# Kernel tuning notes

Measured on AMD Instinct MI355X. Metric: run time of the kernel, lower is better.

## Reference

```python
import jax, jax.numpy as jnp
import numpy as np

B, C, H, W = 4, 64, 256, 256
WIDE = 256      # num_features * width_multiplier
K = 4           # dynamic kernel banks
KS = 3          # kernel size
RED = 16        # channels // reduction = 64 // 4
PAD = KS // 2


def _wn(v, g):
    # torch weight_norm, dim=0: norm over all dims except leading dim
    n = jnp.sqrt(jnp.sum(v * v, axis=tuple(range(1, v.ndim)), keepdims=True))
    return g * v / n


def _conv(x, w, groups=1):
    return jax.lax.conv_general_dilated(
        x, w, window_strides=(1, 1), padding=[(PAD, PAD), (PAD, PAD)],
        feature_group_count=groups, dimension_numbers=('NCHW', 'OIHW', 'NCHW'))


def setup_inputs() -> dict:
    key = jax.random.key(0)
    ks = jax.random.split(key, 16)
    s = lambda k, shape, sc: jax.random.normal(k, shape, jnp.float32) * sc
    return {
        'x': jax.random.normal(ks[0], (B, C, H, W), jnp.float32),
        'scale': jax.random.uniform(ks[1], (B, 1), jnp.float32, 1.0, 4.0),
        # body conv 1 (weight-normed, ReLU)
        'v1': s(ks[2], (WIDE, C, KS, KS), 0.05), 'g1': jnp.ones((WIDE, 1, 1, 1), jnp.float32),
        'b1': jnp.zeros((WIDE,), jnp.float32),
        # body conv 2 (weight-normed, no act)
        'v2': s(ks[3], (C, WIDE, KS, KS), 0.05), 'g2': jnp.ones((C, 1, 1, 1), jnp.float32),
        'b2': jnp.zeros((C,), jnp.float32),
        # scale-aware dynamic conv: K banks of [C_out, C_in, k, k], weight-normed over dim 0 (=K)
        'dyn_v': s(ks[4], (K, C, C, KS, KS), 0.05), 'dyn_g': jnp.ones((K, 1, 1, 1, 1), jnp.float32),
        'dyn_b': jnp.zeros((K, C), jnp.float32),
        # routing: Linear(1 -> K) + softmax
        'att_w': s(ks[5], (1, K), 1.0), 'att_b': jnp.zeros((K,), jnp.float32),
        # SE block: Linear(C -> C/red, no bias), ReLU, Linear(C/red -> C, no bias), Sigmoid
        'se_w1': s(ks[6], (RED, C), 0.1), 'se_w2': s(ks[7], (C, RED), 0.1),
    }


def reference(x, scale, v1, g1, b1, v2, g2, b2, dyn_v, dyn_g, dyn_b,
              att_w, att_b, se_w1, se_w2):
    # --- body: wide weight-normed conv stack ---
    r = jax.nn.relu(_conv(x, _wn(v1, g1)) + b1[None, :, None, None])   # [B,WIDE,H,W]
    r = _conv(r, _wn(v2, g2)) + b2[None, :, None, None]                # [B,C,H,W]
    # --- scale-aware dynamic conv: per-sample softmax mix of K kernels ---
    att = jax.nn.softmax(scale @ att_w + att_b, axis=-1)               # [B,K]
    w_bank = _wn(dyn_v, dyn_g)                                         # [K,C,C,k,k]
    w_b = jnp.einsum('bk,koicd->boicd', att, w_bank)                   # [B,C,C,k,k]
    bias_b = att @ dyn_b                                               # [B,C]
    # batch-grouped conv: one distinct kernel per sample
    y = _conv(r.reshape(1, B * C, H, W), w_b.reshape(B * C, C, KS, KS), groups=B)
    y = y.reshape(B, C, H, W) + bias_b[:, :, None, None]
    # --- SE gating ---
    p = jnp.mean(y, axis=(2, 3))                                       # [B,C]
    gate = jax.nn.sigmoid(jax.nn.relu(p @ se_w1.T) @ se_w2.T)          # [B,C]
    y = y * gate[:, :, None, None]
    # --- residual ---
    return x + y
```

## Files before the change

kernel.cpp:

```cpp
#include <hip/hip_runtime.h>

typedef __attribute__((ext_vector_type(8))) short short8;
typedef __attribute__((ext_vector_type(4))) float f32x4;

#define HH 256
#define WW 256

__device__ inline unsigned int f2bf(float x) {
  unsigned int u = __float_as_uint(x);
  return (u + 0x7fffu + ((u >> 16) & 1u)) >> 16;
}
__device__ inline unsigned int pack2(float a, float b) {
  return f2bf(a) | (f2bf(b) << 16);
}

__global__ __launch_bounds__(256) void xpose_k(const float* __restrict__ x,
                                               unsigned short* __restrict__ xcl) {
  const int t = threadIdx.x;
  const int ci = t & 63;
  const int wv = t >> 6;
  const int x0 = blockIdx.x * 64;
  const int y  = blockIdx.y;
  const int b  = blockIdx.z;
  const float* src = x + ((size_t)(b * 64 + ci) * HH + y) * WW + x0 + wv;
  unsigned short* dst = xcl + ((size_t)(b * HH + y) * WW + x0 + wv) * 64 + ci;
#pragma unroll
  for (int k = 0; k < 16; ++k)
    dst[(size_t)k * 4 * 64] = (unsigned short)f2bf(src[4 * k]);
}

template <int COUT, int CINK>
__global__ __launch_bounds__(256) void wnorm_k(const float* __restrict__ v,
                                               const float* __restrict__ g,
                                               unsigned short* __restrict__ out) {
  constexpr int N = CINK * 9;
  const int co = blockIdx.x, t = threadIdx.x;
  const float* vb = v + (size_t)co * N;
  float s = 0.f;
  for (int i = t; i < N; i += 256) { float a = vb[i]; s += a * a; }
  for (int off = 32; off > 0; off >>= 1) s += __shfl_xor(s, off, 64);
  __shared__ float red[4];
  if ((t & 63) == 0) red[t >> 6] = s;
  __syncthreads();
  const float tot = red[0] + red[1] + red[2] + red[3];
  const float sc = g[co] / sqrtf(tot);
  for (int i = t; i < N; i += 256) {
    int ci = i / 9, tap = i - 9 * (i / 9);
    out[((size_t)tap * COUT + co) * CINK + ci] = (unsigned short)f2bf(vb[i] * sc);
  }
}

__global__ __launch_bounds__(256) void dynnorm_k(const float* __restrict__ dyn_v,
                                                 const float* __restrict__ dyn_g,
                                                 float* __restrict__ dscale) {
  const int k = blockIdx.x, t = threadIdx.x;
  const float* vb = dyn_v + (size_t)k * 36864;
  float s = 0.f;
  for (int i = t; i < 36864; i += 256) { float a = vb[i]; s += a * a; }
  for (int off = 32; off > 0; off >>= 1) s += __shfl_xor(s, off, 64);
  __shared__ float red[4];
  if ((t & 63) == 0) red[t >> 6] = s;
  __syncthreads();
  if (t == 0) dscale[k] = dyn_g[k] / sqrtf(red[0] + red[1] + red[2] + red[3]);
}

__global__ __launch_bounds__(256) void mix_k(const float* __restrict__ scale,
                                             const float* __restrict__ att_w,
                                             const float* __restrict__ att_b,
                                             const float* __restrict__ dyn_v,
                                             const float* __restrict__ dyn_b,
                                             const float* __restrict__ dscale,
                                             unsigned short* __restrict__ wbt,
                                             float* __restrict__ bias_b,
                                             float* __restrict__ zp) {
  const int blk = blockIdx.x;
  const int b = blk >> 6, co = blk & 63;
  const int t = threadIdx.x;
  float att[4], wsc[4];
  const float sc = scale[b];
  float mx = -1e30f;
#pragma unroll
  for (int k = 0; k < 4; ++k) { att[k] = sc * att_w[k] + att_b[k]; mx = fmaxf(mx, att[k]); }
  float den = 0.f;
#pragma unroll
  for (int k = 0; k < 4; ++k) { att[k] = expf(att[k] - mx); den += att[k]; }
#pragma unroll
  for (int k = 0; k < 4; ++k) { att[k] /= den; wsc[k] = att[k] * dscale[k]; }
  for (int i = t; i < 576; i += 256) {
    int ci = i / 9, tap = i - 9 * (i / 9);
    float w = 0.f;
#pragma unroll
    for (int k = 0; k < 4; ++k)
      w += wsc[k] * dyn_v[(((size_t)k * 64 + co) * 64 + ci) * 9 + tap];
    wbt[(((size_t)b * 9 + tap) * 64 + co) * 64 + ci] = (unsigned short)f2bf(w);
  }
  if (t == 0) {
    float bb = 0.f;
#pragma unroll
    for (int k = 0; k < 4; ++k) bb += att[k] * dyn_b[k * 64 + co];
    bias_b[blk] = bb;
  }
  if (blk == 0) zp[t] = 0.f;
}

template <int CIN, int COUT, int OSTR, bool RELU, bool DYN>
__global__ __launch_bounds__(512, 2) void conv3x3_mfma(const unsigned short* __restrict__ in_cl,
                                                       const unsigned short* __restrict__ wt,
                                                       const float* __restrict__ bias,
                                                       unsigned short* __restrict__ out_cl,
                                                       float* __restrict__ y_out,
                                                       float* __restrict__ pblk,
                                                       const float* __restrict__ zp) {
  constexpr int CO_TILES = COUT / 64;
  constexpr int NCH = CIN / 32;
  constexpr int NSLOT = 2448;
  const int tid = threadIdx.x;
  const int lane = tid & 63;
  const int wv = tid >> 6;
  const int l15 = lane & 15;
  const int lg = lane >> 4;

  const int wg = (blockIdx.x & 7) * (gridDim.x >> 3) + (blockIdx.x >> 3);
  int tdec = wg;
  const int cot = tdec % CO_TILES; tdec /= CO_TILES;
  const int bx = tdec & 7; tdec >>= 3;
  const int by = tdec & 15; tdec >>= 4;
  const int bz = tdec;

  const int x0 = bx * 32;
  const int y0 = by * 16;
  const int co0 = cot * 64;

  const unsigned short* inb = in_cl + (size_t)bz * HH * WW * CIN;
  const unsigned short* wtb = wt + (DYN ? (size_t)bz * 9 * 64 * 64 : (size_t)0);
  const float* biasb = bias + (DYN ? bz * 64 : 0);
  const unsigned short* zp16 = (const unsigned short*)zp;

  __shared__ __align__(16) char lds[131072];

  const unsigned short* sptr[5];
#pragma unroll
  for (int k = 0; k < 5; ++k) {
    const int u = k * 512 + tid;
    const int pair = u >> 3;
    const int s = ((u & 7) * 16) ^ ((pair & 7) << 4);
    const int parity = s >> 6;
    const int g = (s >> 4) & 3;
    const int px = 2 * pair + parity;
    const int row = px / 34, col = px - 34 * row;
    const int gy = y0 - 1 + row, gx = x0 - 1 + col;
    const bool ok = (u < NSLOT) && ((unsigned)gy < (unsigned)HH) && ((unsigned)gx < (unsigned)WW);
    sptr[k] = ok ? (inb + ((size_t)(gy * WW + gx)) * CIN + g * 8) : zp16;
  }
  int dyA[2], gA[2], coA[2];
  bool aval[2];
#pragma unroll
  for (int r = 0; r < 2; ++r) {
    const int slot = r * 512 + tid;
    dyA[r] = slot >> 8;
    gA[r] = (slot >> 6) & 3;
    coA[r] = slot & 63;
    aval[r] = (slot < 768);
  }

  f32x4 acc[4][4];
#pragma unroll
  for (int m = 0; m < 4; ++m)
#pragma unroll
    for (int n = 0; n < 4; ++n) acc[m][n] = (f32x4){0.f, 0.f, 0.f, 0.f};

#define STAGE_I(c, IBOFS)                                                          \
  do {                                                                             \
    _Pragma("unroll") for (int k_ = 0; k_ < 5; ++k_)                               \
        __builtin_amdgcn_global_load_lds(                                          \
            (const void*)(sptr[k_] + (c) * 32),                                    \
            (void*)(lds + (IBOFS) + (k_ * 512 + wv * 64) * 16), 16, 0, 0);         \
  } while (0)

#define STAGE_A(d, c, bidx)                                                        \
  do {                                                                             \
    _Pragma("unroll") for (int r_ = 0; r_ < 2; ++r_) {                             \
      const unsigned short* s_ =                                                   \
          aval[r_] ? wtb + ((size_t)((dyA[r_] * 3 + (d)) * COUT + co0 + coA[r_])) * CIN + \
                         (c) * 32 + gA[r_] * 8                                     \
                   : zp16;                                                         \
      __builtin_amdgcn_global_load_lds(                                            \
          (const void*)s_,                                                         \
          (void*)(lds + 81920 + (bidx) * 16384 + (r_ * 512 + wv * 64) * 16), 16, 0, 0); \
    }                                                                              \
  } while (0)

#define PHASE(DXV, IBOFS, WAITN, ...)                                              \
  do {                                                                             \
    short8 Af[3][4], Bv[2][4];                                                     \
    {                                                                              \
      const char* aB_ = lds + 81920 + (DXV) * 16384;                               \
      _Pragma("unroll") for (int dy = 0; dy < 3; ++dy)                             \
          _Pragma("unroll") for (int m = 0; m < 4; ++m)                            \
              Af[dy][m] = *(const short8*)(aB_ + (dy * 4 + lg) * 1024 +            \
                                           (16 * m + l15) * 16);                   \
      const char* iB_ = lds + (IBOFS);                                             \
      _Pragma("unroll") for (int c2 = 0; c2 < 2; ++c2)                             \
          _Pragma("unroll") for (int bi = 0; bi < 4; ++bi) {                       \
        const int px_ = (2 * wv + bi) * 34 + 16 * c2 + l15 + (DXV);                \
        const int by_ = (px_ >> 1) * 128 +                                         \
                        ((lg * 16 + (px_ & 1) * 64) ^ (((px_ >> 1) & 7) << 4));    \
        Bv[c2][bi] = *(const short8*)(iB_ + by_);                                  \
      }                                                                            \
    }                                                                              \
    __VA_ARGS__;                                                                   \
    __builtin_amdgcn_s_setprio(1);                                                 \
    _Pragma("unroll") for (int c2 = 0; c2 < 2; ++c2)                               \
        _Pragma("unroll") for (int bi = 0; bi < 4; ++bi)                           \
            _Pragma("unroll") for (int dy = 0; dy < 3; ++dy) {                     \
      if (dy < ((bi > 1) ? (bi - 1) : 0) || dy > ((bi < 2) ? bi : 2)) continue;    \
      const int n_ = 2 * (bi - dy) + c2;                                           \
      _Pragma("unroll") for (int m = 0; m < 4; ++m)                                \
          acc[m][n_] = __builtin_amdgcn_mfma_f32_16x16x32_bf16(Af[dy][m],          \
                                                               Bv[c2][bi],        \
                                                               acc[m][n_], 0, 0, 0); \
    }                                                                              \
    __builtin_amdgcn_s_setprio(0);                                                 \
    asm volatile("s_waitcnt vmcnt(" #WAITN ")" ::: "memory");                      \
    __builtin_amdgcn_s_barrier();                                                  \
  } while (0)

  STAGE_I(0, 0);
  STAGE_A(0, 0, 0);
  STAGE_A(1, 0, 1);
  asm volatile("s_waitcnt vmcnt(2)" ::: "memory");
  __builtin_amdgcn_s_barrier();

#pragma unroll 1
  for (int ch = 0; ch < NCH - 1; ++ch) {
    const int ib = (ch & 1) * 40960;
    const int ibn = 40960 - ib;
    PHASE(0, ib, 7, STAGE_A(2, ch, 2); STAGE_I(ch + 1, ibn));
    PHASE(1, ib, 7, STAGE_A(0, ch + 1, 0));
    PHASE(2, ib, 2, STAGE_A(1, ch + 1, 1));
  }
  {
    const int ib = ((NCH - 1) & 1) * 40960;
    PHASE(0, ib, 2, STAGE_A(2, NCH - 1, 2));
    PHASE(1, ib, 0, (void)0);
    PHASE(2, ib, 0, (void)0);
  }
#undef PHASE
#undef STAGE_A
#undef STAGE_I

  float scol[4][4];
  if (DYN) {
#pragma unroll
    for (int m = 0; m < 4; ++m)
#pragma unroll
      for (int f = 0; f < 4; ++f) scol[m][f] = 0.f;
  }

#pragma unroll
  for (int m = 0; m < 4; ++m) {
    const f32x4 bs = *(const f32x4*)(biasb + co0 + 16 * m + 4 * lg);
#pragma unroll
    for (int n = 0; n < 4; ++n) {
      f32x4 v = acc[m][n] + bs;
      if (RELU) {
        v.x = fmaxf(v.x, 0.f); v.y = fmaxf(v.y, 0.f);
        v.z = fmaxf(v.z, 0.f); v.w = fmaxf(v.w, 0.f);
      }
      const int yy = y0 + 2 * wv + (n >> 1);
      const int xx = x0 + 16 * (n & 1) + l15;
      if (!DYN) {
        uint2 pk;
        pk.x = pack2(v.x, v.y);
        pk.y = pack2(v.z, v.w);
        *(uint2*)(out_cl + (size_t)bz * HH * WW * OSTR +
                  ((size_t)(yy * WW + xx)) * OSTR + co0 + 16 * m + 4 * lg) = pk;
      } else {
        const size_t base = ((size_t)(bz * 64 + 16 * m + 4 * lg) * HH + yy) * WW + xx;
        y_out[base]             = v.x;
        y_out[base + 1 * 65536] = v.y;
        y_out[base + 2 * 65536] = v.z;
        y_out[base + 3 * 65536] = v.w;
        scol[m][0] += v.x; scol[m][1] += v.y; scol[m][2] += v.z; scol[m][3] += v.w;
      }
    }
  }
  if (DYN) {
#pragma unroll
    for (int m = 0; m < 4; ++m)
#pragma unroll
      for (int f = 0; f < 4; ++f) {
        float r = scol[m][f];
        r += __shfl_xor(r, 1, 64);
        r += __shfl_xor(r, 2, 64);
        r += __shfl_xor(r, 4, 64);
        r += __shfl_xor(r, 8, 64);
        scol[m][f] = r;
      }
    __syncthreads();
    float* red = (float*)lds;
    if (l15 == 0) {
#pragma unroll
      for (int m = 0; m < 4; ++m)
#pragma unroll
        for (int f = 0; f < 4; ++f)
          red[wv * 64 + 16 * m + 4 * lg + f] = scol[m][f];
    }
    __syncthreads();
    if (tid < 64) {
      float s = 0.f;
#pragma unroll
      for (int w = 0; w < 8; ++w) s += red[w * 64 + tid];
      pblk[((size_t)bz * 128 + by * 8 + bx) * 64 + tid] = s;
    }
  }
}

__global__ __launch_bounds__(256) void gate_k(const float* __restrict__ pblk,
                                              const float* __restrict__ se_w1,
                                              const float* __restrict__ se_w2,
                                              float* __restrict__ gate) {
  const int b = blockIdx.x;
  const int t = threadIdx.x;
  const int c = t & 63, part = t >> 6;
  __shared__ float ps[4][64];
  __shared__ float p_s[64], h_s[16];
  float s = 0.f;
  for (int blk = part; blk < 128; blk += 4)
    s += pblk[((size_t)b * 128 + blk) * 64 + c];
  ps[part][c] = s;
  __syncthreads();
  if (t < 64) p_s[t] = (ps[0][t] + ps[1][t] + ps[2][t] + ps[3][t]) * (1.f / 65536.f);
  __syncthreads();
  if (t < 16) {
    float h = 0.f;
    for (int cc = 0; cc < 64; ++cc) h += p_s[cc] * se_w1[t * 64 + cc];
    h_s[t] = fmaxf(h, 0.f);
  }
  __syncthreads();
  if (t < 64) {
    float a = 0.f;
    for (int j = 0; j < 16; ++j) a += h_s[j] * se_w2[t * 16 + j];
    gate[b * 64 + t] = 1.f / (1.f + expf(-a));
  }
}

__global__ __launch_bounds__(256) void final_k(const float* __restrict__ x,
                                               const float* __restrict__ gate,
                                               float* __restrict__ out) {
  const size_t i = ((size_t)blockIdx.x * 256 + threadIdx.x) * 4;
  f32x4 yv = *(f32x4*)(out + i);
  const f32x4 xv = *(const f32x4*)(x + i);
  const float g = gate[(int)(i >> 16)];
  yv = xv + yv * g;
  *(f32x4*)(out + i) = yv;
}

static constexpr size_t SZ_XCL = (size_t)4 * 256 * 256 * 64 * 2;
static constexpr size_t SZ_W   = (size_t)9 * 256 * 64 * 2;
static constexpr size_t SZ_PBLK = (size_t)4 * 128 * 64 * 4;

static constexpr size_t B_XCL = 0;
static constexpr size_t B_R   = B_XCL + SZ_XCL;
static constexpr size_t B_W1T = B_R + 4 * SZ_XCL;
static constexpr size_t B_W2T = B_W1T + SZ_W;
static constexpr size_t B_WBT = B_W2T + SZ_W;
static constexpr size_t B_DSC = B_WBT + SZ_W;
static constexpr size_t B_BB  = B_DSC + 256;
static constexpr size_t B_GT  = B_BB + 1024;
static constexpr size_t B_ZP  = B_GT + 1024;
static constexpr size_t B_PBLK = B_ZP + 1024;
static constexpr size_t WS_BIG = B_PBLK + SZ_PBLK;

extern "C" void kernel_launch(void* const* d_in, const int* in_sizes, int n_in,
                              void* d_out, int out_size, void* d_ws, size_t ws_size,
                              hipStream_t stream) {
  (void)in_sizes; (void)n_in; (void)out_size;
  if (ws_size < WS_BIG) return;

  const float* x     = (const float*)d_in[0];
  const float* scale = (const float*)d_in[1];
  const float* v1    = (const float*)d_in[2];
  const float* g1    = (const float*)d_in[3];
  const float* b1    = (const float*)d_in[4];
  const float* v2    = (const float*)d_in[5];
  const float* g2    = (const float*)d_in[6];
  const float* b2    = (const float*)d_in[7];
  const float* dyn_v = (const float*)d_in[8];
  const float* dyn_g = (const float*)d_in[9];
  const float* dyn_b = (const float*)d_in[10];
  const float* att_w = (const float*)d_in[11];
  const float* att_b = (const float*)d_in[12];
  const float* se_w1 = (const float*)d_in[13];
  const float* se_w2 = (const float*)d_in[14];
  float* out = (float*)d_out;

  char* ws = (char*)d_ws;
  unsigned short* xcl  = (unsigned short*)(ws + B_XCL);
  unsigned short* rbuf = (unsigned short*)(ws + B_R);
  unsigned short* r2   = (unsigned short*)(ws + B_XCL);
  unsigned short* w1t  = (unsigned short*)(ws + B_W1T);
  unsigned short* w2t  = (unsigned short*)(ws + B_W2T);
  unsigned short* wbt  = (unsigned short*)(ws + B_WBT);
  float* dscale = (float*)(ws + B_DSC);
  float* bias_b = (float*)(ws + B_BB);
  float* gate   = (float*)(ws + B_GT);
  float* zp     = (float*)(ws + B_ZP);
  float* pblk   = (float*)(ws + B_PBLK);

  xpose_k<<<dim3(4, 256, 4), 256, 0, stream>>>(x, xcl);
  wnorm_k<256, 64><<<256, 256, 0, stream>>>(v1, g1, w1t);
  wnorm_k<64, 256><<<64, 256, 0, stream>>>(v2, g2, w2t);
  dynnorm_k<<<4, 256, 0, stream>>>(dyn_v, dyn_g, dscale);
  mix_k<<<256, 256, 0, stream>>>(scale, att_w, att_b, dyn_v, dyn_b, dscale, wbt, bias_b, zp);

  conv3x3_mfma<64, 256, 256, true, false><<<2048, 512, 0, stream>>>(
      xcl, w1t, b1, rbuf, nullptr, nullptr, zp);
  conv3x3_mfma<256, 64, 64, false, false><<<512, 512, 0, stream>>>(
      rbuf, w2t, b2, r2, nullptr, nullptr, zp);
  conv3x3_mfma<64, 64, 64, false, true><<<512, 512, 0, stream>>>(
      r2, wbt, bias_b, nullptr, out, pblk, zp);

  gate_k<<<4, 256, 0, stream>>>(pblk, se_w1, se_w2, gate);
  final_k<<<16384, 256, 0, stream>>>(x, gate, out);
}
```

Baseline: 352.7 us.

## Store activations and weights in 32-channel planar blocks for contiguous chunk loads

Changes the channel-last bf16 activation and weight layouts into planes of 32 channels. Each input-channel chunk the conv kernel stages is then a contiguous 64-byte-per-pixel region, instead of a strided slice of a wider pixel row. The producers (transpose, weight norm, dynamic mix, conv epilogue) are updated to write the new layout. This is meant to improve DRAM/cache locality of the per-chunk global-to-LDS loads, at the cost of scattering the epilogue stores across planes.

```diff
diff --git a/kernel.cpp b/kernel.cpp
--- a/kernel.cpp
+++ b/kernel.cpp
@@ -5,6 +5,8 @@
 
 #define HH 256
 #define WW 256
+
+static constexpr size_t PS_IN = (size_t)4 * HH * WW * 32;
 
 __device__ inline unsigned int f2bf(float x) {
   unsigned int u = __float_as_uint(x);
@@ -23,10 +25,11 @@
   const int y  = blockIdx.y;
   const int b  = blockIdx.z;
   const float* src = x + ((size_t)(b * 64 + ci) * HH + y) * WW + x0 + wv;
-  unsigned short* dst = xcl + ((size_t)(b * HH + y) * WW + x0 + wv) * 64 + ci;
+  unsigned short* dst = xcl + (size_t)(ci >> 5) * PS_IN +
+                        ((size_t)((b * HH + y) * WW) + x0 + wv) * 32 + (ci & 31);
 #pragma unroll
   for (int k = 0; k < 16; ++k)
-    dst[(size_t)k * 4 * 64] = (unsigned short)f2bf(src[4 * k]);
+    dst[(size_t)k * 4 * 32] = (unsigned short)f2bf(src[4 * k]);
 }
 
 template <int COUT, int CINK>
@@ -34,6 +37,7 @@
                                                const float* __restrict__ g,
                                                unsigned short* __restrict__ out) {
   constexpr int N = CINK * 9;
+  constexpr size_t APS = (size_t)9 * COUT * 32;
   const int co = blockIdx.x, t = threadIdx.x;
   const float* vb = v + (size_t)co * N;
   float s = 0.f;
@@ -46,7 +50,8 @@
   const float sc = g[co] / sqrtf(tot);
   for (int i = t; i < N; i += 256) {
     int ci = i / 9, tap = i - 9 * (i / 9);
-    out[((size_t)tap * COUT + co) * CINK + ci] = (unsigned short)f2bf(vb[i] * sc);
+    out[(size_t)(ci >> 5) * APS + ((size_t)tap * COUT + co) * 32 + (ci & 31)] =
+        (unsigned short)f2bf(vb[i] * sc);
   }
 }
 
@@ -92,7 +97,8 @@
 #pragma unroll
     for (int k = 0; k < 4; ++k)
       w += wsc[k] * dyn_v[(((size_t)k * 64 + co) * 64 + ci) * 9 + tap];
-    wbt[(((size_t)b * 9 + tap) * 64 + co) * 64 + ci] = (unsigned short)f2bf(w);
+    wbt[(size_t)b * 36864 + (size_t)(ci >> 5) * 18432 + ((size_t)tap * 64 + co) * 32 + (ci & 31)] =
+        (unsigned short)f2bf(w);
   }
   if (t == 0) {
     float bb = 0.f;
@@ -103,7 +109,7 @@
   if (blk == 0) zp[t] = 0.f;
 }
 
-template <int CIN, int COUT, int OSTR, bool RELU, bool DYN>
+template <int CIN, int COUT, bool RELU, bool DYN>
 __global__ __launch_bounds__(512, 2) void conv3x3_mfma(const unsigned short* __restrict__ in_cl,
                                                        const unsigned short* __restrict__ wt,
                                                        const float* __restrict__ bias,
@@ -114,6 +120,7 @@
   constexpr int CO_TILES = COUT / 64;
   constexpr int NCH = CIN / 32;
   constexpr int NSLOT = 2448;
+  constexpr size_t APS = (size_t)9 * COUT * 32;
   const int tid = threadIdx.x;
   const int lane = tid & 63;
   const int wv = tid >> 6;
@@ -131,14 +138,15 @@
   const int y0 = by * 16;
   const int co0 = cot * 64;
 
-  const unsigned short* inb = in_cl + (size_t)bz * HH * WW * CIN;
-  const unsigned short* wtb = wt + (DYN ? (size_t)bz * 9 * 64 * 64 : (size_t)0);
+  const unsigned short* inb = in_cl + (size_t)bz * HH * WW * 32;
+  const unsigned short* wtb = wt + (DYN ? (size_t)bz * NCH * APS : (size_t)0);
   const float* biasb = bias + (DYN ? bz * 64 : 0);
   const unsigned short* zp16 = (const unsigned short*)zp;
 
   __shared__ __align__(16) char lds[131072];
 
   const unsigned short* sptr[5];
+  size_t istep[5];
 #pragma unroll
   for (int k = 0; k < 5; ++k) {
     const int u = k * 512 + tid;
@@ -150,7 +158,8 @@
     const int row = px / 34, col = px - 34 * row;
     const int gy = y0 - 1 + row, gx = x0 - 1 + col;
     const bool ok = (u < NSLOT) && ((unsigned)gy < (unsigned)HH) && ((unsigned)gx < (unsigned)WW);
-    sptr[k] = ok ? (inb + ((size_t)(gy * WW + gx)) * CIN + g * 8) : zp16;
+    sptr[k] = ok ? (inb + ((size_t)(gy * WW + gx)) * 32 + g * 8) : zp16;
+    istep[k] = ok ? PS_IN : 0;
   }
   int dyA[2], gA[2], coA[2];
   bool aval[2];
@@ -173,7 +182,7 @@
   do {                                                                             \
     _Pragma("unroll") for (int k_ = 0; k_ < 5; ++k_)                               \
         __builtin_amdgcn_global_load_lds(                                          \
-            (const void*)(sptr[k_] + (c) * 32),                                    \
+            (const void*)(sptr[k_] + (size_t)(c) * istep[k_]),                     \
             (void*)(lds + (IBOFS) + (k_ * 512 + wv * 64) * 16), 16, 0, 0);         \
   } while (0)
 
@@ -181,8 +190,9 @@
   do {                                                                             \
     _Pragma("unroll") for (int r_ = 0; r_ < 2; ++r_) {                             \
       const unsigned short* s_ =                                                   \
-          aval[r_] ? wtb + ((size_t)((dyA[r_] * 3 + (d)) * COUT + co0 + coA[r_])) * CIN + \
-                         (c) * 32 + gA[r_] * 8                                     \
+          aval[r_] ? wt_base + (size_t)(c) * APS +                                 \
+                         ((size_t)((dyA[r_] * 3 + (d)) * COUT + co0 + coA[r_])) * 32 + \
+                         gA[r_] * 8                                                \
                    : zp16;                                                         \
       __builtin_amdgcn_global_load_lds(                                            \
           (const void*)s_,                                                         \
@@ -225,6 +235,8 @@
     __builtin_amdgcn_s_barrier();                                                  \
   } while (0)
 
+  const unsigned short* wt_base = wtb;
+
   STAGE_I(0, 0);
   STAGE_A(0, 0, 0);
   STAGE_A(1, 0, 1);
@@ -273,8 +285,9 @@
         uint2 pk;
         pk.x = pack2(v.x, v.y);
         pk.y = pack2(v.z, v.w);
-        *(uint2*)(out_cl + (size_t)bz * HH * WW * OSTR +
-                  ((size_t)(yy * WW + xx)) * OSTR + co0 + 16 * m + 4 * lg) = pk;
+        const int co = co0 + 16 * m + 4 * lg;
+        *(uint2*)(out_cl + (size_t)(co >> 5) * PS_IN +
+                  ((size_t)((bz * HH + yy) * WW + xx)) * 32 + (co & 31)) = pk;
       } else {
         const size_t base = ((size_t)(bz * 64 + 16 * m + 4 * lg) * HH + yy) * WW + xx;
         y_out[base]             = v.x;
@@ -414,11 +427,11 @@
   dynnorm_k<<<4, 256, 0, stream>>>(dyn_v, dyn_g, dscale);
   mix_k<<<256, 256, 0, stream>>>(scale, att_w, att_b, dyn_v, dyn_b, dscale, wbt, bias_b, zp);
 
-  conv3x3_mfma<64, 256, 256, true, false><<<2048, 512, 0, stream>>>(
+  conv3x3_mfma<64, 256, true, false><<<2048, 512, 0, stream>>>(
       xcl, w1t, b1, rbuf, nullptr, nullptr, zp);
-  conv3x3_mfma<256, 64, 64, false, false><<<512, 512, 0, stream>>>(
+  conv3x3_mfma<256, 64, false, false><<<512, 512, 0, stream>>>(
       rbuf, w2t, b2, r2, nullptr, nullptr, zp);
-  conv3x3_mfma<64, 64, 64, false, true><<<512, 512, 0, stream>>>(
+  conv3x3_mfma<64, 64, false, true><<<512, 512, 0, stream>>>(
       r2, wbt, bias_b, nullptr, out, pblk, zp);
 
   gate_k<<<4, 256, 0, stream>>>(pblk, se_w1, se_w2, gate);
```

Result: faster. 327.2 us, median of 2 (-7.2%).
